# Optimization experiments

Hardware: AMD Instinct MI355X
Metric: run time of the kernel (lower is better)

Reference implementation:

```python
import jax, jax.numpy as jnp
import numpy as np

B, L = 128, 256          # trees per batch, leaves per tree (perfect binary tree)
V, D, H = 50000, 300, 512  # vocab, word_dim, tree_input_dim == output_dim


def setup_inputs() -> dict:
    key = jax.random.key(0)
    ks = jax.random.split(key, 6)
    token_ids = jax.random.randint(ks[0], (B, L), 0, V)
    scale_e = np.sqrt(3.0 / D).astype(np.float32)  # reset_embedding uniform(-scale, scale)
    emb_table = jax.random.uniform(ks[1], (V, D), jnp.float32, -scale_e, scale_e)
    s = 0.02
    Wx = jax.random.normal(ks[2], (D, 5 * H), jnp.float32) * s  # leaf input -> (i, fl, fr, o, u)
    Ul = jax.random.normal(ks[3], (H, 5 * H), jnp.float32) * s  # left child h
    Ur = jax.random.normal(ks[4], (H, 5 * H), jnp.float32) * s  # right child h
    b = jax.random.normal(ks[5], (5 * H,), jnp.float32) * s
    return {"token_ids": token_ids, "emb_table": emb_table, "Wx": Wx, "Ul": Ul, "Ur": Ur, "b": b}


def _cell(xproj, hl, hr, cl, cr, Ul, Ur, b):
    # Binary tree-LSTM cell (Tai et al., fold-style) with per-child forget gates.
    g = xproj + hl @ Ul + hr @ Ur + b            # [..., 5H]
    i, fl, fr, o, u = jnp.split(g, 5, axis=-1)
    c = jax.nn.sigmoid(i) * jnp.tanh(u) + jax.nn.sigmoid(fl) * cl + jax.nn.sigmoid(fr) * cr
    h = jax.nn.sigmoid(o) * jnp.tanh(c)
    return h, c


def reference(token_ids, emb_table, Wx, Ul, Ur, b):
    # Eval mode: all dropouts are identity.
    x = emb_table[token_ids]                      # [B, L, D] leaf word embeddings
    z = jnp.zeros((B, L, H), x.dtype)             # leaf children states are zero
    h, c = _cell(x @ Wx, z, z, z, z, Ul, Ur, b)   # all leaves at once
    hs = [h]
    # Level-wise bottom-up over the perfect binary tree (internal nodes: inputs=None).
    while h.shape[1] > 1:
        hl, hr = h[:, 0::2], h[:, 1::2]
        cl, cr = c[:, 0::2], c[:, 1::2]
        h, c = _cell(jnp.float32(0.0), hl, hr, cl, cr, Ul, Ur, b)
        hs.append(h)
    # Collected hidden states of all 2L-1 nodes (leaves first, then levels up to root).
    return jnp.concatenate(hs, axis=1)            # [B, 2L-1, H]
```

## Files before the change

kernel.cpp:

```cpp
#include <hip/hip_runtime.h>
#include <hip/hip_bf16.h>
#include <cstdint>

#define BB 128
#define LL 256
#define DD 300
#define HH 512
#define TOUT 511
#define NGATE 2560

typedef __attribute__((ext_vector_type(8))) short bf16x8;
typedef __attribute__((ext_vector_type(4))) float f32x4;

__device__ __forceinline__ float rcpf(float x){ return __builtin_amdgcn_rcpf(x); }
__device__ __forceinline__ float ex2f(float x){ return __builtin_amdgcn_exp2f(x); }
__device__ __forceinline__ float sigf(float x){ return rcpf(1.0f + ex2f(x * -1.44269504f)); }
__device__ __forceinline__ float tanh_fast(float x){ return 1.0f - 2.0f*rcpf(ex2f(x * 2.88539008f) + 1.0f); }

__device__ __forceinline__ void load_lds16(const void* g, void* l) {
  __builtin_amdgcn_global_load_lds(
      (const __attribute__((address_space(1))) unsigned int*)g,
      (__attribute__((address_space(3))) unsigned int*)l, 16, 0, 0);
}

#define VMWAIT(n) asm volatile("s_waitcnt vmcnt(" #n ")" ::: "memory")
#define LGKM0()   asm volatile("s_waitcnt lgkmcnt(0)" ::: "memory")

__global__ __launch_bounds__(256) void prep_weights(
    const float* __restrict__ Wx, const float* __restrict__ Ul, const float* __restrict__ Ur,
    __hip_bfloat16* __restrict__ Wb0t, __hip_bfloat16* __restrict__ Wb1t)
{
  const int z = blockIdx.z;
  const float* src; __hip_bfloat16* dst; int Ksrc, Kdst, koff;
  if (z == 0) { if (blockIdx.x >= 5) return; src = Wx; dst = Wb0t; Ksrc = DD; Kdst = 320; koff = 0; }
  else if (z == 1) { src = Ul; dst = Wb1t; Ksrc = HH; Kdst = 1024; koff = 0; }
  else { src = Ur; dst = Wb1t; Ksrc = HH; Kdst = 1024; koff = 512; }

  __shared__ float t[64][65];
  const int tid = threadIdx.x;
  const int k0 = blockIdx.x * 64;
  const int n0 = blockIdx.y * 64;
  #pragma unroll
  for (int p = 0; p < 16; ++p) {
    int lin = p*256 + tid;
    int ki = lin >> 6, nj = lin & 63;
    t[ki][nj] = (k0 + ki < Ksrc) ? src[(size_t)(k0+ki)*NGATE + n0 + nj] : 0.f;
  }
  __syncthreads();
  #pragma unroll
  for (int p = 0; p < 16; ++p) {
    int lin = p*256 + tid;
    int ni = lin >> 6, kj = lin & 63;
    dst[(size_t)(n0+ni)*Kdst + koff + k0 + kj] = __float2bfloat16(t[kj][ni]);
  }
}

__global__ __launch_bounds__(256) void embed_cvt(
    const int* __restrict__ tok, const float* __restrict__ emb,
    __hip_bfloat16* __restrict__ A0)
{
  int idx = blockIdx.x*256 + threadIdx.x;
  int r  = idx / 40;
  int ck = (idx - r*40) * 8;
  int tk = tok[r];
  const float* erow = emb + (size_t)tk*DD;
  float v[8];
  if (ck + 8 <= DD) {
    float4 lo = *reinterpret_cast<const float4*>(erow + ck);
    float4 hi = *reinterpret_cast<const float4*>(erow + ck + 4);
    v[0]=lo.x; v[1]=lo.y; v[2]=lo.z; v[3]=lo.w;
    v[4]=hi.x; v[5]=hi.y; v[6]=hi.z; v[7]=hi.w;
  } else {
    #pragma unroll
    for (int j = 0; j < 8; ++j) { int k = ck + j; v[j] = (k < DD) ? erow[k] : 0.f; }
  }
  bf16x8 o;
  #pragma unroll
  for (int j = 0; j < 8; ++j)
    o[j] = (short)__bfloat16_as_ushort(__float2bfloat16(v[j]));
  *reinterpret_cast<bf16x8*>(&A0[(size_t)r*320 + ck]) = o;
}

__global__ __launch_bounds__(512, 2) void gemm_l0(
    const __hip_bfloat16* __restrict__ A, const __hip_bfloat16* __restrict__ Wt,
    const float* __restrict__ bias,
    float* __restrict__ out, __hip_bfloat16* __restrict__ hout, float* __restrict__ cout)
{
  constexpr int P  = 4;
  constexpr int NT = 10;
  constexpr int HBYT = 36864;
  constexpr size_t rowK = 640;
  constexpr size_t panStride = 256 * rowK;
  __shared__ __align__(16) char lds[4*HBYT];

  const int tid  = threadIdx.x;
  const int lane = tid & 63;
  const int wid  = tid >> 6;
  const int wm   = wid >> 2;
  const int wn   = wid & 3;
  const int bid  = blockIdx.x;
  const int m    = (bid & 7) + ((bid >> 6) << 3);
  const int s    = (bid >> 3) & 7;
  const int n0   = s * 64;

  const bool isAwave = (wid < 4);
  const char* gsrc[5];
  int ldst0;
  if (isAwave) {
    #pragma unroll
    for (int i = 0; i < 4; ++i) {
      int gi  = wid*4 + i;
      int row = gi*16 + (lane >> 2);
      int cs  = (lane & 3) ^ ((row >> 1) & 3);
      gsrc[i] = (const char*)A + (size_t)m*P*panStride + (size_t)row*rowK + cs*16;
    }
    gsrc[4] = nullptr;
    ldst0 = (wid*4)*1024 + lane*16;
  } else {
    #pragma unroll
    for (int i = 0; i < 5; ++i) {
      int bj   = (wid-4)*5 + i;
      int rowb = bj*16 + (lane >> 2);
      int cs   = (lane & 3) ^ ((rowb >> 1) & 3);
      int grow = (rowb >> 6)*512 + n0 + (rowb & 63);
      gsrc[i] = (const char*)Wt + (size_t)grow*rowK + cs*16;
    }
    ldst0 = 16384 + ((wid-4)*5)*1024 + lane*16;
  }

  f32x4 acc[8][5];
  #pragma unroll
  for (int mf = 0; mf < 8; ++mf)
    #pragma unroll
    for (int g5 = 0; g5 < 5; ++g5)
      acc[mf][g5] = (f32x4){0.f,0.f,0.f,0.f};

  int ts = 0, Tstage = 0;
  auto stage = [&](){
    char* base = lds + (size_t)(Tstage & 3)*HBYT + ldst0;
    const size_t kb = (size_t)ts*64;
    if (isAwave) {
      #pragma unroll
      for (int i = 0; i < 4; ++i) load_lds16(gsrc[i] + kb, base + i*1024);
    } else {
      #pragma unroll
      for (int i = 0; i < 5; ++i) load_lds16(gsrc[i] + kb, base + i*1024);
    }
    ++Tstage;
    if (++ts == NT) {
      ts = 0;
      if (isAwave) {
        #pragma unroll
        for (int i = 0; i < 4; ++i) gsrc[i] += panStride;
      }
    }
  };

  stage(); stage(); stage();

  const int jg = n0 + wn*16 + (lane & 15);
  float bia[5];
  #pragma unroll
  for (int g5 = 0; g5 < 5; ++g5) bia[g5] = bias[g5*HH + jg];

  constexpr int total = P * NT;
  #pragma unroll 1
  for (int p = 0; p < P; ++p) {
    #pragma unroll 1
    for (int t = 0; t < NT; ++t) {
      const int Tc = p*NT + t;
      if (Tc + 3 <= total)      { if (isAwave) VMWAIT(8); else VMWAIT(10); }
      else if (Tc + 2 <= total) { if (isAwave) VMWAIT(4); else VMWAIT(5); }
      else                      { VMWAIT(0); }
      LGKM0();
      __builtin_amdgcn_s_barrier();

      const char* Ab = lds + (size_t)(Tc & 3)*HBYT;
      const char* Bb = Ab + 16384;
      const int q = lane >> 4;

      bf16x8 b[5];
      #pragma unroll
      for (int g5 = 0; g5 < 5; ++g5) {
        int c = g5*64 + wn*16 + (lane & 15);
        b[g5] = *(const bf16x8*)(Bb + c*64 + ((q ^ ((c >> 1) & 3))*16));
      }
      bf16x8 a[4];
      #pragma unroll
      for (int i = 0; i < 4; ++i) {
        int r = wm*128 + i*16 + (lane & 15);
        a[i] = *(const bf16x8*)(Ab + r*64 + ((q ^ ((r >> 1) & 3))*16));
      }
      if (Tstage < total) stage();
      __builtin_amdgcn_sched_barrier(0);
      __builtin_amdgcn_s_setprio(1);
      #pragma unroll
      for (int mf = 0; mf < 4; ++mf)
        #pragma unroll
        for (int g5 = 0; g5 < 5; ++g5)
          acc[mf][g5] = __builtin_amdgcn_mfma_f32_16x16x32_bf16(a[mf], b[g5], acc[mf][g5], 0, 0, 0);
      __builtin_amdgcn_s_setprio(0);

      #pragma unroll
      for (int i = 0; i < 4; ++i) {
        int r = wm*128 + (4+i)*16 + (lane & 15);
        a[i] = *(const bf16x8*)(Ab + r*64 + ((q ^ ((r >> 1) & 3))*16));
      }
      __builtin_amdgcn_sched_barrier(0);
      __builtin_amdgcn_s_setprio(1);
      #pragma unroll
      for (int mf = 0; mf < 4; ++mf)
        #pragma unroll
        for (int g5 = 0; g5 < 5; ++g5)
          acc[4+mf][g5] = __builtin_amdgcn_mfma_f32_16x16x32_bf16(a[mf], b[g5], acc[4+mf][g5], 0, 0, 0);
      __builtin_amdgcn_s_setprio(0);
    }

    const int r0 = (m*P + p) * 256;
    #pragma unroll
    for (int mf = 0; mf < 8; ++mf) {
      #pragma unroll
      for (int v = 0; v < 4; ++v) {
        int rr = r0 + wm*128 + mf*16 + (lane >> 4)*4 + v;
        float gi  = acc[mf][0][v] + bia[0];
        float go  = acc[mf][3][v] + bia[3];
        float gu  = acc[mf][4][v] + bia[4];
        float cc = sigf(gi)*tanh_fast(gu);
        float hh = sigf(go)*tanh_fast(cc);
        int b = rr >> 8;
        int t2 = rr & 255;
        out[((size_t)b*TOUT + t2)*HH + jg] = hh;
        hout[(size_t)rr*HH + jg] = __float2bfloat16(hh);
        cout[(size_t)rr*HH + jg] = cc;
        acc[mf][0][v]=0.f; acc[mf][1][v]=0.f; acc[mf][2][v]=0.f;
        acc[mf][3][v]=0.f; acc[mf][4][v]=0.f;
      }
    }
  }
}

__global__ __launch_bounds__(512, 4) void gemm_cell(
    const __hip_bfloat16* __restrict__ A, const __hip_bfloat16* __restrict__ Wt,
    int K, const float* __restrict__ bias, const float* __restrict__ cprev,
    float* __restrict__ out, __hip_bfloat16* __restrict__ hout, float* __restrict__ cout,
    int lkshift, int sc, int numM)
{
  constexpr int BUFS = 28672;
  __shared__ __align__(16) char lds[2*BUFS];

  const int tid  = threadIdx.x;
  const int lane = tid & 63;
  const int wid  = tid >> 6;
  const int wm   = wid >> 2;
  const int wn   = wid & 3;
  const int bid  = blockIdx.x;
  int m, s;
  if (numM >= 8) { m = (bid & 7) + ((bid >> 6) << 3); s = (bid >> 3) & 7; }
  else           { m = bid % numM;  s = bid / numM; }
  const int r0   = m * 128;
  const int n0   = s * 64;
  const size_t rowK = (size_t)K * 2;

  const char* gsrc[4];
  int gi0 = (wid < 4) ? wid*4 : 16 + (wid-4)*3;
  #pragma unroll
  for (int i = 0; i < 4; ++i) {
    int gi = gi0 + i;
    int row = (gi < 8) ? gi*16 + (lane >> 2) : (gi-8)*16 + (lane >> 2);
    int cs = (lane & 3) ^ ((row >> 1) & 3);
    if (gi < 8) {
      gsrc[i] = (const char*)A + (size_t)(r0 + row)*rowK + cs*16;
    } else {
      int grow = (row >> 6)*512 + n0 + (row & 63);
      gsrc[i] = (const char*)Wt + (size_t)grow*rowK + cs*16;
    }
  }
  const int ldst0 = gi0*1024 + lane*16;

  f32x4 acc[4][5];
  #pragma unroll
  for (int mf = 0; mf < 4; ++mf)
    #pragma unroll
    for (int g5 = 0; g5 < 5; ++g5)
      acc[mf][g5] = (f32x4){0.f,0.f,0.f,0.f};

  const int nk = K >> 5;
  auto stage = [&](int buf, int kt){
    char* base = lds + buf*BUFS + ldst0;
    const size_t kb = (size_t)kt*64;
    if (wid < 4) {
      #pragma unroll
      for (int i = 0; i < 4; ++i) load_lds16(gsrc[i] + kb, base + i*1024);
    } else {
      #pragma unroll
      for (int i = 0; i < 3; ++i) load_lds16(gsrc[i] + kb, base + i*1024);
    }
  };

  stage(0, 0);
  int cur = 0;
  for (int kt = 0; kt < nk; ++kt) {
    if (kt + 1 < nk) {
      stage(cur ^ 1, kt + 1);
      if (wid < 4) VMWAIT(4); else VMWAIT(3);
    } else {
      VMWAIT(0);
    }
    __builtin_amdgcn_s_barrier();

    const char* Ab = lds + cur*BUFS;
    const char* Bb = Ab + 8192;
    const int q = lane >> 4;
    bf16x8 b[5];
    #pragma unroll
    for (int g5 = 0; g5 < 5; ++g5) {
      int c = g5*64 + wn*16 + (lane & 15);
      b[g5] = *(const bf16x8*)(Bb + c*64 + ((q ^ ((c >> 1) & 3))*16));
    }
    __builtin_amdgcn_s_setprio(1);
    #pragma unroll
    for (int mf = 0; mf < 4; ++mf) {
      int r = wm*64 + mf*16 + (lane & 15);
      bf16x8 av = *(const bf16x8*)(Ab + r*64 + ((q ^ ((r >> 1) & 3))*16));
      #pragma unroll
      for (int g5 = 0; g5 < 5; ++g5)
        acc[mf][g5] = __builtin_amdgcn_mfma_f32_16x16x32_bf16(av, b[g5], acc[mf][g5], 0, 0, 0);
    }
    __builtin_amdgcn_s_setprio(0);
    __builtin_amdgcn_s_barrier();
    cur ^= 1;
  }

  const int Lmask = (1 << lkshift) - 1;
  const int jg = n0 + wn*16 + (lane & 15);
  float bia[5];
  #pragma unroll
  for (int g5 = 0; g5 < 5; ++g5) bia[g5] = bias[g5*HH + jg];
  #pragma unroll
  for (int mf = 0; mf < 4; ++mf) {
    #pragma unroll
    for (int v = 0; v < 4; ++v) {
      int rr = r0 + wm*64 + mf*16 + (lane >> 4)*4 + v;
      float gi  = acc[mf][0][v] + bia[0];
      float gfl = acc[mf][1][v] + bia[1];
      float gfr = acc[mf][2][v] + bia[2];
      float go  = acc[mf][3][v] + bia[3];
      float gu  = acc[mf][4][v] + bia[4];
      float cl = cprev[(size_t)(2*rr)*HH + jg];
      float cr = cprev[(size_t)(2*rr)*HH + HH + jg];
      float cc = sigf(gi)*tanh_fast(gu) + sigf(gfl)*cl + sigf(gfr)*cr;
      float hh = sigf(go)*tanh_fast(cc);
      int b = rr >> lkshift;
      int t = rr & Lmask;
      out[((size_t)b*TOUT + sc + t)*HH + jg] = hh;
      hout[(size_t)rr*HH + jg] = __float2bfloat16(hh);
      cout[(size_t)rr*HH + jg] = cc;
    }
  }
}

__global__ __launch_bounds__(512, 2) void gemm_tail(
    const __hip_bfloat16* __restrict__ A, const __hip_bfloat16* __restrict__ Wt,
    const float* __restrict__ bias, const float* __restrict__ cprev,
    float* __restrict__ out, __hip_bfloat16* __restrict__ hout, float* __restrict__ cout,
    int lkshift, int sc, int numM)
{
  constexpr int ABYTES = 16384;
  constexpr int BUFS   = ABYTES + 40960;
  __shared__ __align__(16) char lds[2*BUFS];

  const int tid  = threadIdx.x;
  const int lane = tid & 63;
  const int wid  = tid >> 6;
  const int wm   = wid >> 2;
  const int wn   = wid & 3;
  const int bid  = blockIdx.x;
  int m, s;
  if (numM >= 8) { m = (bid & 7) + ((bid >> 6) << 3); s = (bid >> 3) & 7; }
  else           { m = bid % numM;  s = bid / numM; }
  const int r0   = m * 128;
  const int n0   = s * 64;
  constexpr size_t rowK = 2048;

  const int srow = lane >> 3;
  const int gq   = (lane & 7) ^ srow;
  const char* gsrc[7];
  #pragma unroll
  for (int ii = 0; ii < 7; ++ii) {
    int issue = wid*7 + ii;
    if (issue < 16) {
      int r = issue*8 + srow;
      gsrc[ii] = (const char*)A + (size_t)(r0 + r)*rowK + (size_t)gq*16;
    } else {
      int c = (issue-16)*8 + srow;
      int grow = (c >> 6)*512 + n0 + (c & 63);
      gsrc[ii] = (const char*)Wt + (size_t)grow*rowK + (size_t)gq*16;
    }
  }
  const int ldst0 = (wid*7)*1024 + lane*16;

  f32x4 acc[4][5];
  #pragma unroll
  for (int mf = 0; mf < 4; ++mf)
    #pragma unroll
    for (int g5 = 0; g5 < 5; ++g5)
      acc[mf][g5] = (f32x4){0.f,0.f,0.f,0.f};

  auto stage = [&](int buf, int kt){
    char* base = lds + buf*BUFS + ldst0;
    const size_t kb = (size_t)kt*128;
    #pragma unroll
    for (int ii = 0; ii < 7; ++ii) load_lds16(gsrc[ii] + kb, base + ii*1024);
  };

  stage(0, 0);
  int cur = 0;
  for (int kt = 0; kt < 16; ++kt) {
    if (kt + 1 < 16) {
      stage(cur ^ 1, kt + 1);
      VMWAIT(7);
    } else {
      VMWAIT(0);
    }
    __builtin_amdgcn_s_barrier();

    const char* Ab = lds + cur*BUFS;
    const char* Bb = Ab + ABYTES;
    #pragma unroll
    for (int s2 = 0; s2 < 2; ++s2) {
      const int qb = s2*4 + (lane >> 4);
      bf16x8 b[5];
      #pragma unroll
      for (int g5 = 0; g5 < 5; ++g5) {
        int c = g5*64 + wn*16 + (lane & 15);
        b[g5] = *(const bf16x8*)(Bb + c*128 + ((qb ^ (c & 7))*16));
      }
      __builtin_amdgcn_s_setprio(1);
      #pragma unroll
      for (int mf = 0; mf < 4; ++mf) {
        int r = wm*64 + mf*16 + (lane & 15);
        bf16x8 av = *(const bf16x8*)(Ab + r*128 + ((qb ^ (r & 7))*16));
        #pragma unroll
        for (int g5 = 0; g5 < 5; ++g5)
          acc[mf][g5] = __builtin_amdgcn_mfma_f32_16x16x32_bf16(av, b[g5], acc[mf][g5], 0, 0, 0);
      }
      __builtin_amdgcn_s_setprio(0);
    }
    __builtin_amdgcn_s_barrier();
    cur ^= 1;
  }

  const int Lmask = (1 << lkshift) - 1;
  const int jg = n0 + wn*16 + (lane & 15);
  float bia[5];
  #pragma unroll
  for (int g5 = 0; g5 < 5; ++g5) bia[g5] = bias[g5*HH + jg];
  #pragma unroll
  for (int mf = 0; mf < 4; ++mf) {
    #pragma unroll
    for (int v = 0; v < 4; ++v) {
      int rr = r0 + wm*64 + mf*16 + (lane >> 4)*4 + v;
      float gi  = acc[mf][0][v] + bia[0];
      float gfl = acc[mf][1][v] + bia[1];
      float gfr = acc[mf][2][v] + bia[2];
      float go  = acc[mf][3][v] + bia[3];
      float gu  = acc[mf][4][v] + bia[4];
      float cl = cprev[(size_t)(2*rr)*HH + jg];
      float cr = cprev[(size_t)(2*rr)*HH + HH + jg];
      float cc = sigf(gi)*tanh_fast(gu) + sigf(gfl)*cl + sigf(gfr)*cr;
      float hh = sigf(go)*tanh_fast(cc);
      int b = rr >> lkshift;
      int t = rr & Lmask;
      out[((size_t)b*TOUT + sc + t)*HH + jg] = hh;
      hout[(size_t)rr*HH + jg] = __float2bfloat16(hh);
      cout[(size_t)rr*HH + jg] = cc;
    }
  }
}

extern "C" void kernel_launch(void* const* d_in, const int* in_sizes, int n_in,
                              void* d_out, int out_size, void* d_ws, size_t ws_size,
                              hipStream_t stream) {
  (void)in_sizes; (void)n_in; (void)out_size; (void)ws_size;
  const int*   tok  = (const int*)d_in[0];
  const float* emb  = (const float*)d_in[1];
  const float* Wx   = (const float*)d_in[2];
  const float* Ul   = (const float*)d_in[3];
  const float* Ur   = (const float*)d_in[4];
  const float* bias = (const float*)d_in[5];
  float* out = (float*)d_out;

  char* ws = (char*)d_ws;
  size_t off = 0;
  __hip_bfloat16* Wb0t = (__hip_bfloat16*)(ws + off); off += (size_t)NGATE*320*2;
  __hip_bfloat16* Wb1t = (__hip_bfloat16*)(ws + off); off += (size_t)NGATE*1024*2;
  __hip_bfloat16* hA   = (__hip_bfloat16*)(ws + off); off += (size_t)32768*HH*2;
  __hip_bfloat16* hB   = (__hip_bfloat16*)(ws + off); off += (size_t)16384*HH*2;
  float*          cA   = (float*)(ws + off);          off += (size_t)32768*HH*4;
  float*          cB   = (float*)(ws + off);          off += (size_t)16384*HH*4;
  __hip_bfloat16* A0   = (__hip_bfloat16*)cB;

  prep_weights<<<dim3(8, 40, 3), 256, 0, stream>>>(Wx, Ul, Ur, Wb0t, Wb1t);
  embed_cvt<<<(32768*40)/256, 256, 0, stream>>>(tok, emb, A0);

  gemm_l0<<<256, 512, 0, stream>>>(A0, Wb0t, bias, out, hA, cA);
  gemm_cell<<<(16384/128)*8, 512, 0, stream>>>(hA, Wb1t, 1024, bias, cA,
                                               out, hB, cB, 7, 256, 16384/128);
  gemm_cell<<<(8192/128)*8, 512, 0, stream>>>(hB, Wb1t, 1024, bias, cB,
                                              out, hA, cA, 6, 384, 8192/128);
  for (int k = 3; k <= 8; ++k) {
    int M = 32768 >> k;
    int sc = HH - (HH >> k);
    const __hip_bfloat16* Ain = (k & 1) ? hA : hB;
    __hip_bfloat16*       hO  = (k & 1) ? hB : hA;
    const float*          cI  = (k & 1) ? cA : cB;
    float*                cO  = (k & 1) ? cB : cA;
    int numM = M / 128;
    gemm_tail<<<numM*8, 512, 0, stream>>>(Ain, Wb1t, bias, cI,
                                          out, hO, cO, 8 - k, sc, numM);
  }
}
```

Baseline: 388.4 us.

## Replace persistent leaf GEMM with per-tile 128-row blocks and K=128 double buffering

The leaf-level GEMM used 256 persistent blocks, each looping over four 256-row panels with a 4-deep K=32 pipeline and dedicated A/B loader waves. It now launches 2048 blocks, each computing one 128x320 output tile. All waves load cooperatively with K=128 stages, an XOR swizzle and a two-buffer scheme. This gives more parallelism and fewer barriers per K, in exchange for less A reuse per block, more weight reloads, and larger LDS per block (about 112KB), which limits occupancy.

```diff
diff --git a/kernel.cpp b/kernel.cpp
--- a/kernel.cpp
+++ b/kernel.cpp
@@ -81,17 +81,16 @@
   *reinterpret_cast<bf16x8*>(&A0[(size_t)r*320 + ck]) = o;
 }
 
-__global__ __launch_bounds__(512, 2) void gemm_l0(
+__global__ __launch_bounds__(512, 2) void gemm_tail0(
     const __hip_bfloat16* __restrict__ A, const __hip_bfloat16* __restrict__ Wt,
     const float* __restrict__ bias,
     float* __restrict__ out, __hip_bfloat16* __restrict__ hout, float* __restrict__ cout)
 {
-  constexpr int P  = 4;
-  constexpr int NT = 10;
-  constexpr int HBYT = 36864;
+  constexpr int ABYTES = 16384;
+  constexpr int BUFS   = ABYTES + 40960;
   constexpr size_t rowK = 640;
-  constexpr size_t panStride = 256 * rowK;
-  __shared__ __align__(16) char lds[4*HBYT];
+  constexpr int NK = 5;
+  __shared__ __align__(16) char lds[2*BUFS];
 
   const int tid  = threadIdx.x;
   const int lane = tid & 63;
@@ -101,140 +100,96 @@
   const int bid  = blockIdx.x;
   const int m    = (bid & 7) + ((bid >> 6) << 3);
   const int s    = (bid >> 3) & 7;
+  const int r0   = m * 128;
   const int n0   = s * 64;
 
-  const bool isAwave = (wid < 4);
-  const char* gsrc[5];
-  int ldst0;
-  if (isAwave) {
-    #pragma unroll
-    for (int i = 0; i < 4; ++i) {
-      int gi  = wid*4 + i;
-      int row = gi*16 + (lane >> 2);
-      int cs  = (lane & 3) ^ ((row >> 1) & 3);
-      gsrc[i] = (const char*)A + (size_t)m*P*panStride + (size_t)row*rowK + cs*16;
-    }
-    gsrc[4] = nullptr;
-    ldst0 = (wid*4)*1024 + lane*16;
-  } else {
-    #pragma unroll
-    for (int i = 0; i < 5; ++i) {
-      int bj   = (wid-4)*5 + i;
-      int rowb = bj*16 + (lane >> 2);
-      int cs   = (lane & 3) ^ ((rowb >> 1) & 3);
-      int grow = (rowb >> 6)*512 + n0 + (rowb & 63);
-      gsrc[i] = (const char*)Wt + (size_t)grow*rowK + cs*16;
-    }
-    ldst0 = 16384 + ((wid-4)*5)*1024 + lane*16;
-  }
-
-  f32x4 acc[8][5];
-  #pragma unroll
-  for (int mf = 0; mf < 8; ++mf)
+  const int srow = lane >> 3;
+  const int gq   = (lane & 7) ^ srow;
+  const char* gsrc[7];
+  #pragma unroll
+  for (int ii = 0; ii < 7; ++ii) {
+    int issue = wid*7 + ii;
+    if (issue < 16) {
+      int r = issue*8 + srow;
+      gsrc[ii] = (const char*)A + (size_t)(r0 + r)*rowK + (size_t)gq*16;
+    } else {
+      int c = (issue-16)*8 + srow;
+      int grow = (c >> 6)*512 + n0 + (c & 63);
+      gsrc[ii] = (const char*)Wt + (size_t)grow*rowK + (size_t)gq*16;
+    }
+  }
+  const int ldst0 = (wid*7)*1024 + lane*16;
+
+  f32x4 acc[4][5];
+  #pragma unroll
+  for (int mf = 0; mf < 4; ++mf)
     #pragma unroll
     for (int g5 = 0; g5 < 5; ++g5)
       acc[mf][g5] = (f32x4){0.f,0.f,0.f,0.f};
 
-  int ts = 0, Tstage = 0;
-  auto stage = [&](){
-    char* base = lds + (size_t)(Tstage & 3)*HBYT + ldst0;
-    const size_t kb = (size_t)ts*64;
-    if (isAwave) {
-      #pragma unroll
-      for (int i = 0; i < 4; ++i) load_lds16(gsrc[i] + kb, base + i*1024);
-    } else {
-      #pragma unroll
-      for (int i = 0; i < 5; ++i) load_lds16(gsrc[i] + kb, base + i*1024);
-    }
-    ++Tstage;
-    if (++ts == NT) {
-      ts = 0;
-      if (isAwave) {
+  auto stage = [&](int buf, int kt){
+    char* base = lds + buf*BUFS + ldst0;
+    const size_t kb = (size_t)kt*128;
+    #pragma unroll
+    for (int ii = 0; ii < 7; ++ii) load_lds16(gsrc[ii] + kb, base + ii*1024);
+  };
+
+  stage(0, 0);
+  int cur = 0;
+  for (int kt = 0; kt < NK; ++kt) {
+    if (kt + 1 < NK) {
+      stage(cur ^ 1, kt + 1);
+      VMWAIT(7);
+    } else {
+      VMWAIT(0);
+    }
+    __builtin_amdgcn_s_barrier();
+
+    const char* Ab = lds + cur*BUFS;
+    const char* Bb = Ab + ABYTES;
+    #pragma unroll
+    for (int s2 = 0; s2 < 2; ++s2) {
+      const int qb = s2*4 + (lane >> 4);
+      bf16x8 b[5];
+      #pragma unroll
+      for (int g5 = 0; g5 < 5; ++g5) {
+        int c = g5*64 + wn*16 + (lane & 15);
+        b[g5] = *(const bf16x8*)(Bb + c*128 + ((qb ^ (c & 7))*16));
+      }
+      __builtin_amdgcn_s_setprio(1);
+      #pragma unroll
+      for (int mf = 0; mf < 4; ++mf) {
+        int r = wm*64 + mf*16 + (lane & 15);
+        bf16x8 av = *(const bf16x8*)(Ab + r*128 + ((qb ^ (r & 7))*16));
         #pragma unroll
-        for (int i = 0; i < 4; ++i) gsrc[i] += panStride;
+        for (int g5 = 0; g5 < 5; ++g5)
+          acc[mf][g5] = __builtin_amdgcn_mfma_f32_16x16x32_bf16(av, b[g5], acc[mf][g5], 0, 0, 0);
       }
-    }
-  };
-
-  stage(); stage(); stage();
+      __builtin_amdgcn_s_setprio(0);
+    }
+    __builtin_amdgcn_s_barrier();
+    cur ^= 1;
+  }
 
   const int jg = n0 + wn*16 + (lane & 15);
   float bia[5];
   #pragma unroll
   for (int g5 = 0; g5 < 5; ++g5) bia[g5] = bias[g5*HH + jg];
-
-  constexpr int total = P * NT;
-  #pragma unroll 1
-  for (int p = 0; p < P; ++p) {
-    #pragma unroll 1
-    for (int t = 0; t < NT; ++t) {
-      const int Tc = p*NT + t;
-      if (Tc + 3 <= total)      { if (isAwave) VMWAIT(8); else VMWAIT(10); }
-      else if (Tc + 2 <= total) { if (isAwave) VMWAIT(4); else VMWAIT(5); }
-      else                      { VMWAIT(0); }
-      LGKM0();
-      __builtin_amdgcn_s_barrier();
-
-      const char* Ab = lds + (size_t)(Tc & 3)*HBYT;
-      const char* Bb = Ab + 16384;
-      const int q = lane >> 4;
-
-      bf16x8 b[5];
-      #pragma unroll
-      for (int g5 = 0; g5 < 5; ++g5) {
-        int c = g5*64 + wn*16 + (lane & 15);
-        b[g5] = *(const bf16x8*)(Bb + c*64 + ((q ^ ((c >> 1) & 3))*16));
-      }
-      bf16x8 a[4];
-      #pragma unroll
-      for (int i = 0; i < 4; ++i) {
-        int r = wm*128 + i*16 + (lane & 15);
-        a[i] = *(const bf16x8*)(Ab + r*64 + ((q ^ ((r >> 1) & 3))*16));
-      }
-      if (Tstage < total) stage();
-      __builtin_amdgcn_sched_barrier(0);
-      __builtin_amdgcn_s_setprio(1);
-      #pragma unroll
-      for (int mf = 0; mf < 4; ++mf)
-        #pragma unroll
-        for (int g5 = 0; g5 < 5; ++g5)
-          acc[mf][g5] = __builtin_amdgcn_mfma_f32_16x16x32_bf16(a[mf], b[g5], acc[mf][g5], 0, 0, 0);
-      __builtin_amdgcn_s_setprio(0);
-
-      #pragma unroll
-      for (int i = 0; i < 4; ++i) {
-        int r = wm*128 + (4+i)*16 + (lane & 15);
-        a[i] = *(const bf16x8*)(Ab + r*64 + ((q ^ ((r >> 1) & 3))*16));
-      }
-      __builtin_amdgcn_sched_barrier(0);
-      __builtin_amdgcn_s_setprio(1);
-      #pragma unroll
-      for (int mf = 0; mf < 4; ++mf)
-        #pragma unroll
-        for (int g5 = 0; g5 < 5; ++g5)
-          acc[4+mf][g5] = __builtin_amdgcn_mfma_f32_16x16x32_bf16(a[mf], b[g5], acc[4+mf][g5], 0, 0, 0);
-      __builtin_amdgcn_s_setprio(0);
-    }
-
-    const int r0 = (m*P + p) * 256;
-    #pragma unroll
-    for (int mf = 0; mf < 8; ++mf) {
-      #pragma unroll
-      for (int v = 0; v < 4; ++v) {
-        int rr = r0 + wm*128 + mf*16 + (lane >> 4)*4 + v;
-        float gi  = acc[mf][0][v] + bia[0];
-        float go  = acc[mf][3][v] + bia[3];
-        float gu  = acc[mf][4][v] + bia[4];
-        float cc = sigf(gi)*tanh_fast(gu);
-        float hh = sigf(go)*tanh_fast(cc);
-        int b = rr >> 8;
-        int t2 = rr & 255;
-        out[((size_t)b*TOUT + t2)*HH + jg] = hh;
-        hout[(size_t)rr*HH + jg] = __float2bfloat16(hh);
-        cout[(size_t)rr*HH + jg] = cc;
-        acc[mf][0][v]=0.f; acc[mf][1][v]=0.f; acc[mf][2][v]=0.f;
-        acc[mf][3][v]=0.f; acc[mf][4][v]=0.f;
-      }
+  #pragma unroll
+  for (int mf = 0; mf < 4; ++mf) {
+    #pragma unroll
+    for (int v = 0; v < 4; ++v) {
+      int rr = r0 + wm*64 + mf*16 + (lane >> 4)*4 + v;
+      float gi  = acc[mf][0][v] + bia[0];
+      float go  = acc[mf][3][v] + bia[3];
+      float gu  = acc[mf][4][v] + bia[4];
+      float cc = sigf(gi)*tanh_fast(gu);
+      float hh = sigf(go)*tanh_fast(cc);
+      int b = rr >> 8;
+      int t = rr & 255;
+      out[((size_t)b*TOUT + t)*HH + jg] = hh;
+      hout[(size_t)rr*HH + jg] = __float2bfloat16(hh);
+      cout[(size_t)rr*HH + jg] = cc;
     }
   }
 }
@@ -503,7 +458,7 @@
   prep_weights<<<dim3(8, 40, 3), 256, 0, stream>>>(Wx, Ul, Ur, Wb0t, Wb1t);
   embed_cvt<<<(32768*40)/256, 256, 0, stream>>>(tok, emb, A0);
 
-  gemm_l0<<<256, 512, 0, stream>>>(A0, Wb0t, bias, out, hA, cA);
+  gemm_tail0<<<2048, 512, 0, stream>>>(A0, Wb0t, bias, out, hA, cA);
   gemm_cell<<<(16384/128)*8, 512, 0, stream>>>(hA, Wb1t, 1024, bias, cA,
                                                out, hB, cB, 7, 256, 16384/128);
   gemm_cell<<<(8192/128)*8, 512, 0, stream>>>(hB, Wb1t, 1024, bias, cB,
```

Measured after the change: 397.2 us. 2.2% more time.
